# Kernel optimization log

Hardware: AMD Instinct MI355X
Metric: run time of the kernel (lower is better)

Reference implementation:

```python
import jax, jax.numpy as jnp
import numpy as np

N = 8192      # num nodes
D = 256       # input feature dim (num_embeddings)
F_OUT = 128   # out_channels
B = 4096      # lookup batch size


def setup_inputs() -> dict:
    key = jax.random.key(0)
    k1, k2, k3, k4 = jax.random.split(key, 4)
    x = jax.random.randint(k1, (B,), 0, N)                      # node ids for final lookup
    adj = jax.random.randint(k2, (N, N), 0, 2).astype(jnp.int32)  # dense 0/1 adjacency
    embedding = jax.random.normal(k3, (N, D), dtype=jnp.float32)
    xavier = 1.414 * (6.0 / (D + F_OUT)) ** 0.5
    W = jax.random.uniform(k4, (D, F_OUT), minval=-xavier, maxval=xavier, dtype=jnp.float32)
    return {"x": x, "adj": adj, "embedding": embedding, "W": W}


def reference(x, adj, embedding, W):
    Wh = embedding @ W                                   # [N, F_OUT]
    mask = adj > 0
    maskf = mask.astype(Wh.dtype)
    # per-row neighbor mean of Wh (vectorized form of the python row loop)
    deg = jnp.maximum(jnp.sum(maskf, axis=1), 1.0)       # guard; random adj has deg>0
    neigh_mean = (maskf @ Wh) / deg[:, None]             # [N, F_OUT]
    alpha = jnp.sum(Wh * neigh_mean, axis=1)             # [N], Wh[i] . mean(neighbors)
    e = Wh @ Wh.T + alpha[:, None]                       # similarity + row-wise query term
    att = jax.nn.softmax(jnp.where(mask, e, jnp.asarray(-9e15, e.dtype)), axis=1)
    # dropout is identity in eval mode (p effectively 0)
    h_prime = att @ Wh                                   # [N, F_OUT]
    emb_out = jax.nn.elu(h_prime)                        # concat=True branch
    out = emb_out[x]                                     # F.embedding lookup, [B, F_OUT]
    nrm = jnp.linalg.norm(out, axis=1, keepdims=True)
    return out / jnp.maximum(nrm, 1e-12)                 # F.normalize (L2, eps=1e-12)
```

## Files before the change

kernel.cpp:

```cpp
#include <hip/hip_runtime.h>

#define NN 8192
#define DD 256
#define FF 128
#define BB 4096
#define NSPLIT 8
#define KCHUNK (NN / NSPLIT)
#define NITER (KCHUNK / 64)

typedef unsigned short ushortT;
typedef __attribute__((ext_vector_type(8))) short bf16x8;
typedef __attribute__((ext_vector_type(4))) float f32x4;

__device__ __forceinline__ ushortT f2bf(float f) {
  unsigned u = __float_as_uint(f);
  return (ushortT)((u + 0x7FFFu + ((u >> 16) & 1u)) >> 16);
}
__device__ __forceinline__ float bf2f(ushortT h) {
  return __uint_as_float(((unsigned)h) << 16);
}


__global__ __launch_bounds__(256) void init_kernel(int* flags, int* cnt) {
  int i = blockIdx.x * 256 + threadIdx.x;
  flags[i] = 0;
  if (i == 0) *cnt = 0;
}

__global__ __launch_bounds__(256) void scatter_kernel(const int* __restrict__ x, int* flags) {
  int b = blockIdx.x * 256 + threadIdx.x;
  flags[x[b]] = 1;
}

__global__ __launch_bounds__(256) void compact_kernel(const int* __restrict__ flags, int* cnt,
                                                      int* list, int* slot) {
  int i = blockIdx.x * 256 + threadIdx.x;
  if (flags[i]) {
    int pos = atomicAdd(cnt, 1);
    list[pos] = i;
    slot[i] = pos;
  }
}


__global__ __launch_bounds__(256) void pack_kernel(const int* __restrict__ adj,
                                                   const int* __restrict__ list,
                                                   const int* __restrict__ cntp,
                                                   unsigned* __restrict__ pk) {
  const int s = blockIdx.x >> 2;
  const int kc = (blockIdx.x & 3) * 2048;
  if (s >= *cntp) return;
  const int w = threadIdx.x >> 6, l = threadIdx.x & 63;
  const int* base = adj + (size_t)list[s] * NN + kc + w * 512;
  unsigned long long* dst = (unsigned long long*)(pk + s * 256 + (kc >> 5) + w * 16);
#pragma unroll
  for (int i = 0; i < 8; ++i) {
    unsigned long long b = __ballot(base[i * 64 + l] > 0);
    if (l == 0) dst[i] = b;
  }
}


__global__ __launch_bounds__(256) void wh_kernel(const float* __restrict__ emb,
                                                 const float* __restrict__ W,
                                                 ushortT* __restrict__ Whh,
                                                 ushortT* __restrict__ Whl) {
  __shared__ float Es[32 * 65];
  __shared__ float Ws[64 * 128];
  const int t = threadIdx.x;
  const int r0 = blockIdx.x * 32;
  const int rg = t >> 5;
  const int cg = t & 31;
  float4 acc[4] = {{0,0,0,0},{0,0,0,0},{0,0,0,0},{0,0,0,0}};
  for (int kc = 0; kc < DD; kc += 64) {
    __syncthreads();
    for (int i = 0; i < 8; ++i) {
      int idx = t + 256 * i;
      int r = idx >> 6, k = idx & 63;
      Es[r * 65 + k] = emb[(r0 + r) * DD + kc + k];
    }
    for (int i = 0; i < 8; ++i) {
      int idx = t + 256 * i;
      int kr = idx >> 5, c4 = (idx & 31) * 4;
      *(float4*)&Ws[kr * 128 + c4] = *(const float4*)&W[(kc + kr) * 128 + c4];
    }
    __syncthreads();
    for (int k = 0; k < 64; ++k) {
      float4 b = *(const float4*)&Ws[k * 128 + cg * 4];
#pragma unroll
      for (int i = 0; i < 4; ++i) {
        float a = Es[(rg * 4 + i) * 65 + k];
        acc[i].x += a * b.x; acc[i].y += a * b.y;
        acc[i].z += a * b.z; acc[i].w += a * b.w;
      }
    }
  }
#pragma unroll
  for (int i = 0; i < 4; ++i) {
    int row = r0 + rg * 4 + i;
    float v[4] = {acc[i].x, acc[i].y, acc[i].z, acc[i].w};
    ushort4 hh, ll;
    ushortT* hp = (ushortT*)&hh;
    ushortT* lp = (ushortT*)&ll;
#pragma unroll
    for (int k = 0; k < 4; ++k) {
      ushortT h = f2bf(v[k]);
      hp[k] = h;
      lp[k] = f2bf(v[k] - bf2f(h));
    }
    *(ushort4*)&Whh[row * FF + cg * 4] = hh;
    *(ushort4*)&Whl[row * FF + cg * 4] = ll;
  }
}


__global__ __launch_bounds__(256) void transpose_kernel(const ushortT* __restrict__ A,
                                                        ushortT* __restrict__ At) {
  __shared__ ushortT tile[64 * 72];
  const int t = threadIdx.x;
  const int r0 = (blockIdx.x >> 1) * 64, c0 = (blockIdx.x & 1) * 64;
#pragma unroll
  for (int i = 0; i < 2; ++i) {
    int idx = t + 256 * i;
    int r = idx >> 3, cb = idx & 7;
    *(bf16x8*)&tile[r * 72 + ((cb ^ ((r >> 3) & 7)) * 8)] =
        *(const bf16x8*)&A[(size_t)(r0 + r) * FF + c0 + cb * 8];
  }
  __syncthreads();
#pragma unroll
  for (int i = 0; i < 2; ++i) {
    int idx = t + 256 * i;
    int f = idx >> 3, r8 = idx & 7;
    bf16x8 v;
#pragma unroll
    for (int u = 0; u < 8; ++u) {
      int row = r8 * 8 + u;
      v[u] = (short)tile[row * 72 + (((f >> 3) ^ ((row >> 3) & 7)) * 8) + (f & 7)];
    }
    *(bf16x8*)&At[(size_t)(c0 + f) * NN + r0 + r8 * 8] = v;
  }
}


__global__ __launch_bounds__(256) void attn_kernel(
    const ushortT* __restrict__ Whh, const ushortT* __restrict__ Whl,
    const ushortT* __restrict__ WhT, const unsigned* __restrict__ pk,
    const int* __restrict__ list, const int* __restrict__ cntp,
    float* __restrict__ Opart, float* __restrict__ mpart, float* __restrict__ lpart) {
  __shared__ short Kh[2][64 * 128];
  __shared__ short Kl[2][64 * 128];
  __shared__ short Ps[4][16 * 72];
  __shared__ int nid[64];

  const int cnt = *cntp;
  const int qblk = blockIdx.x >> 3, chunk = blockIdx.x & 7;
  const int q0 = qblk * 64;
  if (q0 >= cnt) return;

  const int t = threadIdx.x;
  if (t < 64) nid[t] = list[min(q0 + t, cnt - 1)];
  __syncthreads();

  const int w = t >> 6, l = t & 63, quad = l >> 4, c = l & 15;

  const size_t qr = (size_t)nid[w * 16 + c] * FF;
  bf16x8 qh[4], ql[4];
#pragma unroll
  for (int ks = 0; ks < 4; ++ks) {
    qh[ks] = *(const bf16x8*)(Whh + qr + ks * 32 + quad * 8);
    ql[ks] = *(const bf16x8*)(Whl + qr + ks * 32 + quad * 8);
  }
  int prow[4];
#pragma unroll
  for (int r = 0; r < 4; ++r) prow[r] = min(q0 + w * 16 + quad * 4 + r, cnt - 1);

  float m[4], lr[4];
#pragma unroll
  for (int r = 0; r < 4; ++r) { m[r] = -1e30f; lr[r] = 0.f; }
  f32x4 O[8] = {{0,0,0,0},{0,0,0,0},{0,0,0,0},{0,0,0,0},
                {0,0,0,0},{0,0,0,0},{0,0,0,0},{0,0,0,0}};

  const int kt0 = chunk * KCHUNK;

  bf16x8 sgh[4], sgl[4];
  {
    const ushortT* gh = Whh + (size_t)kt0 * FF;
    const ushortT* gl = Whl + (size_t)kt0 * FF;
#pragma unroll
    for (int i = 0; i < 4; ++i) {
      int idx = t + 256 * i;
      sgh[i] = *(const bf16x8*)(gh + idx * 8);
      sgl[i] = *(const bf16x8*)(gl + idx * 8);
    }
#pragma unroll
    for (int i = 0; i < 4; ++i) {
      int idx = t + 256 * i;
      int r = idx >> 4, cb = idx & 15;
      int off = r * 128 + ((cb ^ (r & 7)) * 8);
      *(bf16x8*)&Kh[0][off] = sgh[i];
      *(bf16x8*)&Kl[0][off] = sgl[i];
    }
  }

  for (int it = 0; it < NITER; ++it) {
    const int kt = kt0 + it * 64;
    const int cur = it & 1;
    if (it + 1 < NITER) {
      const ushortT* gh = Whh + (size_t)(kt + 64) * FF;
      const ushortT* gl = Whl + (size_t)(kt + 64) * FF;
#pragma unroll
      for (int i = 0; i < 4; ++i) {
        int idx = t + 256 * i;
        sgh[i] = *(const bf16x8*)(gh + idx * 8);
        sgl[i] = *(const bf16x8*)(gl + idx * 8);
      }
    }
    unsigned mw0[4], mw1[4];
#pragma unroll
    for (int r = 0; r < 4; ++r) {
      uint2 mm = *(const uint2*)(pk + (size_t)prow[r] * 256 + (kt >> 5));
      mw0[r] = mm.x; mw1[r] = mm.y;
    }
    __syncthreads();

    f32x4 sacc[4];
#pragma unroll
    for (int nt = 0; nt < 4; ++nt) {
      const int rb = (nt * 16 + c) * 128;
      f32x4 a = {0, 0, 0, 0};
#pragma unroll
      for (int ks = 0; ks < 4; ++ks) {
        const int off = rb + (((ks * 4 + quad) ^ (c & 7)) * 8);
        bf16x8 bh = *(const bf16x8*)&Kh[cur][off];
        bf16x8 bl = *(const bf16x8*)&Kl[cur][off];
        a = __builtin_amdgcn_mfma_f32_16x16x32_bf16(qh[ks], bh, a, 0, 0, 0);
        a = __builtin_amdgcn_mfma_f32_16x16x32_bf16(ql[ks], bh, a, 0, 0, 0);
        a = __builtin_amdgcn_mfma_f32_16x16x32_bf16(qh[ks], bl, a, 0, 0, 0);
      }
      sacc[nt] = a;
    }

    float rmax[4];
#pragma unroll
    for (int r = 0; r < 4; ++r) {
      float v = -1e30f;
#pragma unroll
      for (int nt = 0; nt < 4; ++nt) {
        unsigned bit = ((nt < 2 ? mw0[r] : mw1[r]) >> ((nt & 1) * 16 + c)) & 1u;
        v = fmaxf(v, bit ? sacc[nt][r] : -1e30f);
      }
      rmax[r] = v;
    }
#pragma unroll
    for (int mk = 1; mk <= 8; mk <<= 1)
#pragma unroll
      for (int r = 0; r < 4; ++r) rmax[r] = fmaxf(rmax[r], __shfl_xor(rmax[r], mk, 16));
    float sc[4], psum[4];
#pragma unroll
    for (int r = 0; r < 4; ++r) {
      float nm = fmaxf(m[r], rmax[r]);
      sc[r] = __expf(m[r] - nm);
      m[r] = nm;
      psum[r] = 0.f;
    }
#pragma unroll
    for (int nt = 0; nt < 4; ++nt)
#pragma unroll
      for (int r = 0; r < 4; ++r) {
        unsigned bit = ((nt < 2 ? mw0[r] : mw1[r]) >> ((nt & 1) * 16 + c)) & 1u;
        float p = bit ? __expf(sacc[nt][r] - m[r]) : 0.f;
        ushortT pb = f2bf(p);
        Ps[w][(quad * 4 + r) * 72 + nt * 16 + c] = (short)pb;
        psum[r] += bf2f(pb);
      }
#pragma unroll
    for (int mk = 1; mk <= 8; mk <<= 1)
#pragma unroll
      for (int r = 0; r < 4; ++r) psum[r] += __shfl_xor(psum[r], mk, 16);
#pragma unroll
    for (int r = 0; r < 4; ++r) lr[r] = lr[r] * sc[r] + psum[r];

#pragma unroll
    for (int ft = 0; ft < 8; ++ft)
#pragma unroll
      for (int r = 0; r < 4; ++r) O[ft][r] *= sc[r];
    bf16x8 pa[2];
#pragma unroll
    for (int ks2 = 0; ks2 < 2; ++ks2)
      pa[ks2] = *(const bf16x8*)&Ps[w][c * 72 + ks2 * 32 + quad * 8];
#pragma unroll
    for (int ft = 0; ft < 8; ++ft) {
      const ushortT* vp = WhT + (size_t)(ft * 16 + c) * NN + kt + quad * 8;
#pragma unroll
      for (int ks2 = 0; ks2 < 2; ++ks2) {
        bf16x8 vb = *(const bf16x8*)(vp + ks2 * 32);
        O[ft] = __builtin_amdgcn_mfma_f32_16x16x32_bf16(pa[ks2], vb, O[ft], 0, 0, 0);
      }
    }

    if (it + 1 < NITER) {
#pragma unroll
      for (int i = 0; i < 4; ++i) {
        int idx = t + 256 * i;
        int r = idx >> 4, cb = idx & 15;
        int off = r * 128 + ((cb ^ (r & 7)) * 8);
        *(bf16x8*)&Kh[1 - cur][off] = sgh[i];
        *(bf16x8*)&Kl[1 - cur][off] = sgl[i];
      }
    }
  }

  float* Op = Opart + (size_t)chunk * 4096 * FF;
#pragma unroll
  for (int ft = 0; ft < 8; ++ft)
#pragma unroll
    for (int r = 0; r < 4; ++r)
      Op[(size_t)(q0 + w * 16 + quad * 4 + r) * FF + ft * 16 + c] = O[ft][r];
  if (c == 0) {
#pragma unroll
    for (int r = 0; r < 4; ++r) {
      mpart[chunk * 4096 + q0 + w * 16 + quad * 4 + r] = m[r];
      lpart[chunk * 4096 + q0 + w * 16 + quad * 4 + r] = lr[r];
    }
  }
}


__global__ __launch_bounds__(128) void combine_kernel(
    const float* __restrict__ Opart, const float* __restrict__ mpart,
    const float* __restrict__ lpart, float* __restrict__ h) {
  const int r = blockIdx.x;
  const int t = threadIdx.x;
  float mstar = -1e30f;
#pragma unroll
  for (int c = 0; c < NSPLIT; ++c) mstar = fmaxf(mstar, mpart[c * 4096 + r]);
  float lstar = 0.f, acc = 0.f;
#pragma unroll
  for (int c = 0; c < NSPLIT; ++c) {
    float wgt = __expf(mpart[c * 4096 + r] - mstar);
    lstar += wgt * lpart[c * 4096 + r];
    acc += wgt * Opart[((size_t)c * 4096 + r) * FF + t];
  }
  float v = acc / fmaxf(lstar, 1e-30f);
  h[r * FF + t] = v > 0.f ? v : expm1f(v);
}


__global__ __launch_bounds__(128) void out_kernel(const int* __restrict__ x,
                                                  const int* __restrict__ slot,
                                                  const float* __restrict__ h,
                                                  float* __restrict__ out) {
  const int b = blockIdx.x, t = threadIdx.x;
  const int s = slot[x[b]];
  float v = h[s * FF + t];
  float ss = v * v;
#pragma unroll
  for (int wd = 1; wd <= 32; wd <<= 1) ss += __shfl_xor(ss, wd);
  __shared__ float red[2];
  if ((t & 63) == 0) red[t >> 6] = ss;
  __syncthreads();
  float tot = red[0] + red[1];
  float scale = 1.f / fmaxf(sqrtf(tot), 1e-12f);
  out[b * FF + t] = v * scale;
}


extern "C" void kernel_launch(void* const* d_in, const int* in_sizes, int n_in,
                              void* d_out, int out_size, void* d_ws, size_t ws_size,
                              hipStream_t stream) {
  const int*   x   = (const int*)d_in[0];
  const int*   adj = (const int*)d_in[1];
  const float* emb = (const float*)d_in[2];
  const float* W   = (const float*)d_in[3];
  float* out = (float*)d_out;

  char* base = (char*)d_ws;
  ushortT* Whh = (ushortT*)(base);
  ushortT* Whl = (ushortT*)(base + 2097152);
  float*   h   = (float*)(base + 2097152);
  ushortT* WhT = (ushortT*)(base + 4194304);
  float* Opart = (float*)(base + 6291456);
  float* mpart = (float*)(base + 23068672);
  float* lpart = (float*)(base + 23199744);
  unsigned* pk = (unsigned*)(base + 23330816);
  int*   flags = (int*)(base + 27525120);
  int*   list  = (int*)(base + 27557888);
  int*   slot  = (int*)(base + 27574272);
  int*   cnt   = (int*)(base + 27607040);
  (void)in_sizes; (void)n_in; (void)out_size; (void)ws_size;

  hipLaunchKernelGGL(init_kernel,      dim3(NN / 256), dim3(256), 0, stream, flags, cnt);
  hipLaunchKernelGGL(scatter_kernel,   dim3(BB / 256), dim3(256), 0, stream, x, flags);
  hipLaunchKernelGGL(compact_kernel,   dim3(NN / 256), dim3(256), 0, stream, flags, cnt, list, slot);
  hipLaunchKernelGGL(pack_kernel,      dim3(4096 * 4), dim3(256), 0, stream, adj, list, cnt, pk);
  hipLaunchKernelGGL(wh_kernel,        dim3(NN / 32),  dim3(256), 0, stream, emb, W, Whh, Whl);
  hipLaunchKernelGGL(transpose_kernel, dim3((NN / 64) * 2), dim3(256), 0, stream, Whh, WhT);
  hipLaunchKernelGGL(attn_kernel,      dim3((BB / 64) * NSPLIT), dim3(256), 0, stream,
                     Whh, Whl, WhT, pk, list, cnt, Opart, mpart, lpart);
  hipLaunchKernelGGL(combine_kernel,   dim3(4096), dim3(128), 0, stream, Opart, mpart, lpart, h);
  hipLaunchKernelGGL(out_kernel,       dim3(BB),   dim3(128), 0, stream, x, slot, h, out);
}
```

Measured before the change: 461.0 us.

## Drop LDS K staging, read keys from global, double split-K chunks

The attention kernel no longer stages the high and low bf16 key tiles through double-buffered shared memory. Each wave now reads its key fragments straight from global memory, which removes the LDS stores and the per-iteration barrier. The key dimension is split into 16 chunks instead of 8 to launch more blocks, a launch_bounds occupancy hint is added, and the workspace offsets are moved to fit the larger partial-output buffer. In exchange, the four waves of a block each fetch the same key rows from global or cache, and the combine step has twice as many partials to merge.

```diff
diff --git a/kernel.cpp b/kernel.cpp
--- a/kernel.cpp
+++ b/kernel.cpp
@@ -4,7 +4,7 @@
 #define DD 256
 #define FF 128
 #define BB 4096
-#define NSPLIT 8
+#define NSPLIT 16
 #define KCHUNK (NN / NSPLIT)
 #define NITER (KCHUNK / 64)
 
@@ -142,18 +142,16 @@
 }
 
 
-__global__ __launch_bounds__(256) void attn_kernel(
+__global__ __launch_bounds__(256, 3) void attn_kernel(
     const ushortT* __restrict__ Whh, const ushortT* __restrict__ Whl,
     const ushortT* __restrict__ WhT, const unsigned* __restrict__ pk,
     const int* __restrict__ list, const int* __restrict__ cntp,
     float* __restrict__ Opart, float* __restrict__ mpart, float* __restrict__ lpart) {
-  __shared__ short Kh[2][64 * 128];
-  __shared__ short Kl[2][64 * 128];
   __shared__ short Ps[4][16 * 72];
   __shared__ int nid[64];
 
   const int cnt = *cntp;
-  const int qblk = blockIdx.x >> 3, chunk = blockIdx.x & 7;
+  const int qblk = blockIdx.x >> 4, chunk = blockIdx.x & 15;
   const int q0 = qblk * 64;
   if (q0 >= cnt) return;
 
@@ -182,57 +180,26 @@
 
   const int kt0 = chunk * KCHUNK;
 
-  bf16x8 sgh[4], sgl[4];
-  {
-    const ushortT* gh = Whh + (size_t)kt0 * FF;
-    const ushortT* gl = Whl + (size_t)kt0 * FF;
-#pragma unroll
-    for (int i = 0; i < 4; ++i) {
-      int idx = t + 256 * i;
-      sgh[i] = *(const bf16x8*)(gh + idx * 8);
-      sgl[i] = *(const bf16x8*)(gl + idx * 8);
-    }
-#pragma unroll
-    for (int i = 0; i < 4; ++i) {
-      int idx = t + 256 * i;
-      int r = idx >> 4, cb = idx & 15;
-      int off = r * 128 + ((cb ^ (r & 7)) * 8);
-      *(bf16x8*)&Kh[0][off] = sgh[i];
-      *(bf16x8*)&Kl[0][off] = sgl[i];
-    }
-  }
-
   for (int it = 0; it < NITER; ++it) {
     const int kt = kt0 + it * 64;
-    const int cur = it & 1;
-    if (it + 1 < NITER) {
-      const ushortT* gh = Whh + (size_t)(kt + 64) * FF;
-      const ushortT* gl = Whl + (size_t)(kt + 64) * FF;
-#pragma unroll
-      for (int i = 0; i < 4; ++i) {
-        int idx = t + 256 * i;
-        sgh[i] = *(const bf16x8*)(gh + idx * 8);
-        sgl[i] = *(const bf16x8*)(gl + idx * 8);
-      }
-    }
+
     unsigned mw0[4], mw1[4];
 #pragma unroll
     for (int r = 0; r < 4; ++r) {
       uint2 mm = *(const uint2*)(pk + (size_t)prow[r] * 256 + (kt >> 5));
       mw0[r] = mm.x; mw1[r] = mm.y;
     }
-    __syncthreads();
 
     f32x4 sacc[4];
 #pragma unroll
     for (int nt = 0; nt < 4; ++nt) {
-      const int rb = (nt * 16 + c) * 128;
+      const ushortT* kh = Whh + (size_t)(kt + nt * 16 + c) * FF + quad * 8;
+      const ushortT* kl = Whl + (size_t)(kt + nt * 16 + c) * FF + quad * 8;
       f32x4 a = {0, 0, 0, 0};
 #pragma unroll
       for (int ks = 0; ks < 4; ++ks) {
-        const int off = rb + (((ks * 4 + quad) ^ (c & 7)) * 8);
-        bf16x8 bh = *(const bf16x8*)&Kh[cur][off];
-        bf16x8 bl = *(const bf16x8*)&Kl[cur][off];
+        bf16x8 bh = *(const bf16x8*)(kh + ks * 32);
+        bf16x8 bl = *(const bf16x8*)(kl + ks * 32);
         a = __builtin_amdgcn_mfma_f32_16x16x32_bf16(qh[ks], bh, a, 0, 0, 0);
         a = __builtin_amdgcn_mfma_f32_16x16x32_bf16(ql[ks], bh, a, 0, 0, 0);
         a = __builtin_amdgcn_mfma_f32_16x16x32_bf16(qh[ks], bl, a, 0, 0, 0);
@@ -295,17 +262,6 @@
       for (int ks2 = 0; ks2 < 2; ++ks2) {
         bf16x8 vb = *(const bf16x8*)(vp + ks2 * 32);
         O[ft] = __builtin_amdgcn_mfma_f32_16x16x32_bf16(pa[ks2], vb, O[ft], 0, 0, 0);
-      }
-    }
-
-    if (it + 1 < NITER) {
-#pragma unroll
-      for (int i = 0; i < 4; ++i) {
-        int idx = t + 256 * i;
-        int r = idx >> 4, cb = idx & 15;
-        int off = r * 128 + ((cb ^ (r & 7)) * 8);
-        *(bf16x8*)&Kh[1 - cur][off] = sgh[i];
-        *(bf16x8*)&Kl[1 - cur][off] = sgl[i];
       }
     }
   }
@@ -380,13 +336,13 @@
   float*   h   = (float*)(base + 2097152);
   ushortT* WhT = (ushortT*)(base + 4194304);
   float* Opart = (float*)(base + 6291456);
-  float* mpart = (float*)(base + 23068672);
-  float* lpart = (float*)(base + 23199744);
-  unsigned* pk = (unsigned*)(base + 23330816);
-  int*   flags = (int*)(base + 27525120);
-  int*   list  = (int*)(base + 27557888);
-  int*   slot  = (int*)(base + 27574272);
-  int*   cnt   = (int*)(base + 27607040);
+  float* mpart = (float*)(base + 39845888);
+  float* lpart = (float*)(base + 40108032);
+  unsigned* pk = (unsigned*)(base + 40370176);
+  int*   flags = (int*)(base + 44564480);
+  int*   list  = (int*)(base + 44597248);
+  int*   slot  = (int*)(base + 44613632);
+  int*   cnt   = (int*)(base + 44646400);
   (void)in_sizes; (void)n_in; (void)out_size; (void)ws_size;
 
   hipLaunchKernelGGL(init_kernel,      dim3(NN / 256), dim3(256), 0, stream, flags, cnt);
```

After: 578.8 us. 1.26x slower.
